# Kernel optimization log

Measured on AMD Instinct MI355X. Metric: run time of the kernel, lower is better.

The kernel has to match this reference:

```python
import jax, jax.numpy as jnp
import numpy as np

B, H, N, D = 4, 4, 2048, 64

def setup_inputs() -> dict:
    key = jax.random.key(0)
    kq, kk, kv, km = jax.random.split(key, 4)
    q = jax.random.normal(kq, (B, H, N, D), dtype=jnp.float32)
    k = jax.random.normal(kk, (B, H, N, D), dtype=jnp.float32)
    v = jax.random.normal(kv, (B, H, N, D), dtype=jnp.float32)
    mask = jax.random.randint(km, (B, N), 0, 2, dtype=jnp.int32)
    return {"q": q, "k": k, "v": v, "mask": mask}

def reference(q, k, v, mask):
    # scores: [B, H, Nq, Nk]
    scale = jnp.asarray(q.shape[-1] ** 0.5, q.dtype)
    scores = jnp.einsum('bhid,bhjd->bhij', q, k) / scale
    neg = jnp.finfo(scores.dtype).min
    m = mask[:, None, None, :]  # [B,1,1,Nk]
    scores = jnp.where(m == 0, neg, scores)
    attention = jax.nn.softmax(scores, axis=-1)
    output = jnp.einsum('bhij,bhjd->bhid', attention, v)
    return (output, attention)
```

## Files before the change

### kernel.cpp

```cpp
#include <hip/hip_runtime.h>

typedef __attribute__((ext_vector_type(8))) short short8;
typedef __attribute__((ext_vector_type(4))) float f32x4;

#define NHEADS 16
#define N_ 2048
#define D_ 64
#define ROWS 16
#define LDP 2056
#define NT 256

__device__ __forceinline__ unsigned short f2b(float f) {
    unsigned u = __float_as_uint(f);
    return (unsigned short)((u + 0x7FFFu + ((u >> 16) & 1u)) >> 16);
}
__device__ __forceinline__ float b2f(unsigned short b) {
    return __uint_as_float(((unsigned)b) << 16);
}

__global__ __launch_bounds__(NT)
void cvt_bf16_kernel(const float4* __restrict__ src, ushort4* __restrict__ dst, int n4)
{
    int i = blockIdx.x * NT + threadIdx.x;
    if (i < n4) {
        float4 v = src[i];
        ushort4 o;
        o.x = f2b(v.x); o.y = f2b(v.y); o.z = f2b(v.z); o.w = f2b(v.w);
        dst[i] = o;
    }
}

__global__ __launch_bounds__(NT)
void vtrans_kernel(const float* __restrict__ v, unsigned short* __restrict__ vt)
{
    __shared__ float tile[64][65];
    const int head = blockIdx.x >> 5;
    const int k0   = (blockIdx.x & 31) * 64;
    const int tid  = threadIdx.x;

    {
        const int i = tid >> 2;
        const int c = tid & 3;
        const float4* v4 = (const float4*)(v + ((size_t)(head * N_ + k0 + i)) * D_);
        #pragma unroll
        for (int u = 0; u < 4; ++u) {
            const int c4 = c + 4 * u;
            float4 val = v4[c4];
            tile[i][c4 * 4 + 0] = val.x;
            tile[i][c4 * 4 + 1] = val.y;
            tile[i][c4 * 4 + 2] = val.z;
            tile[i][c4 * 4 + 3] = val.w;
        }
    }
    __syncthreads();
    {
        const int d  = tid >> 2;
        const int kk = (tid & 3) * 16;
        unsigned short* dst = vt + ((size_t)(head * D_ + d)) * N_ + k0 + kk;
        #pragma unroll
        for (int m4 = 0; m4 < 4; ++m4) {
            ushort4 ov;
            ov.x = f2b(tile[kk + m4 * 4 + 0][d]);
            ov.y = f2b(tile[kk + m4 * 4 + 1][d]);
            ov.z = f2b(tile[kk + m4 * 4 + 2][d]);
            ov.w = f2b(tile[kk + m4 * 4 + 3][d]);
            *(ushort4*)(dst + m4 * 4) = ov;
        }
    }
}

__global__ __launch_bounds__(NT, 2)
void lg_attn(const unsigned short* __restrict__ Qb,
             const unsigned short* __restrict__ Kb,
             const unsigned short* __restrict__ Vt,
             const int* __restrict__ mask,
             float* __restrict__ out,
             float* __restrict__ attn)
{
    __shared__ unsigned short P[ROWS * LDP];
    __shared__ float wred[64];
    __shared__ float rowinv[ROWS];

    const int tid  = threadIdx.x;
    const int w    = tid >> 6;
    const int lane = tid & 63;
    const int quad = lane >> 4;
    const int l16  = lane & 15;

    const int head = blockIdx.x >> 7;
    const int it   = blockIdx.x & 127;
    const int i0   = it * ROWS;
    const int bidx = head >> 2;

    const unsigned short* qrow = Qb + ((size_t)(head * N_ + i0 + l16)) * D_ + quad * 8;
    const short8 a0 = *(const short8*)qrow;
    const short8 a1 = *(const short8*)(qrow + 32);

    const unsigned short* kbase = Kb + (size_t)head * N_ * D_;
    const int* mrow = mask + bidx * N_;

    float bm[4];
    {
        float m4[4] = {-3.4e38f, -3.4e38f, -3.4e38f, -3.4e38f};
        for (int t = 0; t < 32; ++t) {
            const int j0 = (w + 4 * t) * 16;
            const unsigned short* krow = kbase + (size_t)(j0 + l16) * D_ + quad * 8;
            short8 b0 = *(const short8*)krow;
            short8 b1 = *(const short8*)(krow + 32);
            f32x4 c = {0.f, 0.f, 0.f, 0.f};
            c = __builtin_amdgcn_mfma_f32_16x16x32_bf16(a0, b0, c, 0, 0, 0);
            c = __builtin_amdgcn_mfma_f32_16x16x32_bf16(a1, b1, c, 0, 0, 0);
            const int mv = mrow[j0 + l16];
            #pragma unroll
            for (int r = 0; r < 4; ++r) {
                float s = (mv == 0) ? -3.4e38f : c[r] * 0.125f;
                m4[r] = fmaxf(m4[r], s);
            }
        }
        #pragma unroll
        for (int r = 0; r < 4; ++r) {
            #pragma unroll
            for (int off = 1; off < 16; off <<= 1)
                m4[r] = fmaxf(m4[r], __shfl_xor(m4[r], off, 64));
        }
        if (l16 == 0) {
            #pragma unroll
            for (int r = 0; r < 4; ++r) wred[w * 16 + quad * 4 + r] = m4[r];
        }
        __syncthreads();
        #pragma unroll
        for (int r = 0; r < 4; ++r) {
            const int row = quad * 4 + r;
            bm[r] = fmaxf(fmaxf(wred[row], wred[16 + row]),
                          fmaxf(wred[32 + row], wred[48 + row]));
        }
        __syncthreads();
    }

    {
        float s4[4] = {0.f, 0.f, 0.f, 0.f};
        for (int t = 0; t < 32; ++t) {
            const int j0 = (w + 4 * t) * 16;
            const unsigned short* krow = kbase + (size_t)(j0 + l16) * D_ + quad * 8;
            short8 b0 = *(const short8*)krow;
            short8 b1 = *(const short8*)(krow + 32);
            f32x4 c = {0.f, 0.f, 0.f, 0.f};
            c = __builtin_amdgcn_mfma_f32_16x16x32_bf16(a0, b0, c, 0, 0, 0);
            c = __builtin_amdgcn_mfma_f32_16x16x32_bf16(a1, b1, c, 0, 0, 0);
            const int mv = mrow[j0 + l16];
            #pragma unroll
            for (int r = 0; r < 4; ++r) {
                float s = (mv == 0) ? -3.4e38f : c[r] * 0.125f;
                float p = __expf(s - bm[r]);
                s4[r] += p;
                P[(quad * 4 + r) * LDP + j0 + l16] = f2b(p);
            }
        }
        #pragma unroll
        for (int r = 0; r < 4; ++r) {
            #pragma unroll
            for (int off = 1; off < 16; off <<= 1)
                s4[r] += __shfl_xor(s4[r], off, 64);
        }
        if (l16 == 0) {
            #pragma unroll
            for (int r = 0; r < 4; ++r) wred[w * 16 + quad * 4 + r] = s4[r];
        }
        __syncthreads();
        if (w == 0 && l16 == 0) {
            #pragma unroll
            for (int r = 0; r < 4; ++r) {
                const int row = quad * 4 + r;
                const float bs = wred[row] + wred[16 + row] + wred[32 + row] + wred[48 + row];
                rowinv[row] = 1.0f / bs;
            }
        }
        __syncthreads();
    }

    for (int r = 0; r < ROWS; ++r) {
        const float inv = rowinv[r];
        float4* arow = (float4*)(attn + ((size_t)(head * N_ + i0 + r)) * N_);
        for (int c4 = tid; c4 < N_ / 4; c4 += NT) {
            ushort4 tv = *(ushort4*)&P[r * LDP + c4 * 4];
            float4 f;
            f.x = b2f(tv.x) * inv;
            f.y = b2f(tv.y) * inv;
            f.z = b2f(tv.z) * inv;
            f.w = b2f(tv.w) * inv;
            arow[c4] = f;
            tv.x = f2b(f.x); tv.y = f2b(f.y); tv.z = f2b(f.z); tv.w = f2b(f.w);
            *(ushort4*)&P[r * LDP + c4 * 4] = tv;
        }
    }
    __syncthreads();

    {
        const int n0 = w * 16;
        const unsigned short* vbase =
            Vt + ((size_t)(head * D_ + n0 + l16)) * N_ + quad * 8;
        f32x4 o = {0.f, 0.f, 0.f, 0.f};
        for (int kc = 0; kc < 64; ++kc) {
            short8 ap = *(short8*)&P[l16 * LDP + kc * 32 + quad * 8];
            short8 bv = *(const short8*)(vbase + kc * 32);
            o = __builtin_amdgcn_mfma_f32_16x16x32_bf16(ap, bv, o, 0, 0, 0);
        }
        #pragma unroll
        for (int r = 0; r < 4; ++r)
            out[((size_t)(head * N_ + i0 + quad * 4 + r)) * D_ + n0 + l16] = o[r];
    }
}

extern "C" void kernel_launch(void* const* d_in, const int* in_sizes, int n_in,
                              void* d_out, int out_size, void* d_ws, size_t ws_size,
                              hipStream_t stream) {
    const float* q    = (const float*)d_in[0];
    const float* k    = (const float*)d_in[1];
    const float* v    = (const float*)d_in[2];
    const int*   mask = (const int*)d_in[3];

    float* out  = (float*)d_out;
    float* attn = out + (size_t)NHEADS * N_ * D_;

    const size_t elems = (size_t)NHEADS * N_ * D_;
    unsigned short* Qb = (unsigned short*)d_ws;
    unsigned short* Kb = Qb + elems;
    unsigned short* Vt = Kb + elems;

    const int n4 = (int)(elems / 4);
    const int cblocks = (n4 + NT - 1) / NT;
    cvt_bf16_kernel<<<cblocks, NT, 0, stream>>>((const float4*)q, (ushort4*)Qb, n4);
    cvt_bf16_kernel<<<cblocks, NT, 0, stream>>>((const float4*)k, (ushort4*)Kb, n4);
    vtrans_kernel<<<NHEADS * 32, NT, 0, stream>>>(v, Vt);

    lg_attn<<<NHEADS * 128, NT, 0, stream>>>(Qb, Kb, Vt, mask, out, attn);
}
```

Measured before the change: 458.8 us.

## Keep QK scores in registers to avoid recomputing, defer normalization to output

QK^T scores are computed once and held in 32 f32x4 register tiles instead of being recomputed in a second pass. This removes the second round of K loads and MFMAs. The row-sum reduction goes to a separate slice of shared memory, which drops a barrier and the rowinv step. Normalization of the PV output is deferred to the final store, so P no longer needs to be rewritten, and the attention matrix is written with nontemporal stores. Holding 128 extra VGPRs per thread raises register pressure and may reduce occupancy below the two blocks per CU requested by the launch bounds.

```diff
diff --git a/kernel.cpp b/kernel.cpp
--- a/kernel.cpp
+++ b/kernel.cpp
@@ -78,8 +78,7 @@
              float* __restrict__ attn)
 {
     __shared__ unsigned short P[ROWS * LDP];
-    __shared__ float wred[64];
-    __shared__ float rowinv[ROWS];
+    __shared__ float wred[128];
 
     const int tid  = threadIdx.x;
     const int w    = tid >> 6;
@@ -99,30 +98,39 @@
     const unsigned short* kbase = Kb + (size_t)head * N_ * D_;
     const int* mrow = mask + bidx * N_;
 
-    float bm[4];
-    {
-        float m4[4] = {-3.4e38f, -3.4e38f, -3.4e38f, -3.4e38f};
-        for (int t = 0; t < 32; ++t) {
+    f32x4 c[32];
+    #pragma unroll
+    for (int tc = 0; tc < 4; ++tc) {
+        #pragma unroll
+        for (int ti = 0; ti < 8; ++ti) {
+            const int t  = tc * 8 + ti;
             const int j0 = (w + 4 * t) * 16;
             const unsigned short* krow = kbase + (size_t)(j0 + l16) * D_ + quad * 8;
             short8 b0 = *(const short8*)krow;
             short8 b1 = *(const short8*)(krow + 32);
-            f32x4 c = {0.f, 0.f, 0.f, 0.f};
-            c = __builtin_amdgcn_mfma_f32_16x16x32_bf16(a0, b0, c, 0, 0, 0);
-            c = __builtin_amdgcn_mfma_f32_16x16x32_bf16(a1, b1, c, 0, 0, 0);
+            f32x4 cc = {0.f, 0.f, 0.f, 0.f};
+            cc = __builtin_amdgcn_mfma_f32_16x16x32_bf16(a0, b0, cc, 0, 0, 0);
+            cc = __builtin_amdgcn_mfma_f32_16x16x32_bf16(a1, b1, cc, 0, 0, 0);
             const int mv = mrow[j0 + l16];
             #pragma unroll
-            for (int r = 0; r < 4; ++r) {
-                float s = (mv == 0) ? -3.4e38f : c[r] * 0.125f;
-                m4[r] = fmaxf(m4[r], s);
-            }
-        }
-        #pragma unroll
-        for (int r = 0; r < 4; ++r) {
+            for (int r = 0; r < 4; ++r)
+                c[t][r] = (mv == 0) ? -3.4e38f : cc[r];
+        }
+        __builtin_amdgcn_sched_barrier(0);
+    }
+
+    float bm[4];
+    {
+        float m4[4] = {-3.4e38f, -3.4e38f, -3.4e38f, -3.4e38f};
+        #pragma unroll
+        for (int t = 0; t < 32; ++t)
+            #pragma unroll
+            for (int r = 0; r < 4; ++r) m4[r] = fmaxf(m4[r], c[t][r]);
+        #pragma unroll
+        for (int r = 0; r < 4; ++r)
             #pragma unroll
             for (int off = 1; off < 16; off <<= 1)
                 m4[r] = fmaxf(m4[r], __shfl_xor(m4[r], off, 64));
-        }
         if (l16 == 0) {
             #pragma unroll
             for (int r = 0; r < 4; ++r) wred[w * 16 + quad * 4 + r] = m4[r];
@@ -134,80 +142,70 @@
             bm[r] = fmaxf(fmaxf(wred[row], wred[16 + row]),
                           fmaxf(wred[32 + row], wred[48 + row]));
         }
-        __syncthreads();
     }
 
     {
         float s4[4] = {0.f, 0.f, 0.f, 0.f};
+        #pragma unroll
         for (int t = 0; t < 32; ++t) {
             const int j0 = (w + 4 * t) * 16;
-            const unsigned short* krow = kbase + (size_t)(j0 + l16) * D_ + quad * 8;
-            short8 b0 = *(const short8*)krow;
-            short8 b1 = *(const short8*)(krow + 32);
-            f32x4 c = {0.f, 0.f, 0.f, 0.f};
-            c = __builtin_amdgcn_mfma_f32_16x16x32_bf16(a0, b0, c, 0, 0, 0);
-            c = __builtin_amdgcn_mfma_f32_16x16x32_bf16(a1, b1, c, 0, 0, 0);
-            const int mv = mrow[j0 + l16];
             #pragma unroll
             for (int r = 0; r < 4; ++r) {
-                float s = (mv == 0) ? -3.4e38f : c[r] * 0.125f;
-                float p = __expf(s - bm[r]);
+                const float p = __expf((c[t][r] - bm[r]) * 0.125f);
                 s4[r] += p;
                 P[(quad * 4 + r) * LDP + j0 + l16] = f2b(p);
             }
         }
         #pragma unroll
-        for (int r = 0; r < 4; ++r) {
+        for (int r = 0; r < 4; ++r)
             #pragma unroll
             for (int off = 1; off < 16; off <<= 1)
                 s4[r] += __shfl_xor(s4[r], off, 64);
-        }
         if (l16 == 0) {
             #pragma unroll
-            for (int r = 0; r < 4; ++r) wred[w * 16 + quad * 4 + r] = s4[r];
+            for (int r = 0; r < 4; ++r) wred[64 + w * 16 + quad * 4 + r] = s4[r];
         }
         __syncthreads();
-        if (w == 0 && l16 == 0) {
-            #pragma unroll
-            for (int r = 0; r < 4; ++r) {
-                const int row = quad * 4 + r;
-                const float bs = wred[row] + wred[16 + row] + wred[32 + row] + wred[48 + row];
-                rowinv[row] = 1.0f / bs;
+    }
+
+    {
+        const size_t abase = (size_t)(head * N_ + i0) * N_;
+        #pragma unroll 1
+        for (int r = 0; r < ROWS; ++r) {
+            const float s = wred[64 + r] + wred[80 + r] + wred[96 + r] + wred[112 + r];
+            const float inv = 1.0f / s;
+            f32x4* arow = (f32x4*)(attn + abase + (size_t)r * N_);
+            #pragma unroll
+            for (int u = 0; u < 2; ++u) {
+                const int c4 = tid + u * NT;
+                ushort4 tv = *(ushort4*)&P[r * LDP + c4 * 4];
+                f32x4 f;
+                f.x = b2f(tv.x) * inv;
+                f.y = b2f(tv.y) * inv;
+                f.z = b2f(tv.z) * inv;
+                f.w = b2f(tv.w) * inv;
+                __builtin_nontemporal_store(f, &arow[c4]);
             }
         }
-        __syncthreads();
-    }
-
-    for (int r = 0; r < ROWS; ++r) {
-        const float inv = rowinv[r];
-        float4* arow = (float4*)(attn + ((size_t)(head * N_ + i0 + r)) * N_);
-        for (int c4 = tid; c4 < N_ / 4; c4 += NT) {
-            ushort4 tv = *(ushort4*)&P[r * LDP + c4 * 4];
-            float4 f;
-            f.x = b2f(tv.x) * inv;
-            f.y = b2f(tv.y) * inv;
-            f.z = b2f(tv.z) * inv;
-            f.w = b2f(tv.w) * inv;
-            arow[c4] = f;
-            tv.x = f2b(f.x); tv.y = f2b(f.y); tv.z = f2b(f.z); tv.w = f2b(f.w);
-            *(ushort4*)&P[r * LDP + c4 * 4] = tv;
-        }
-    }
-    __syncthreads();
+    }
 
     {
         const int n0 = w * 16;
         const unsigned short* vbase =
             Vt + ((size_t)(head * D_ + n0 + l16)) * N_ + quad * 8;
         f32x4 o = {0.f, 0.f, 0.f, 0.f};
+        #pragma unroll 4
         for (int kc = 0; kc < 64; ++kc) {
             short8 ap = *(short8*)&P[l16 * LDP + kc * 32 + quad * 8];
             short8 bv = *(const short8*)(vbase + kc * 32);
             o = __builtin_amdgcn_mfma_f32_16x16x32_bf16(ap, bv, o, 0, 0, 0);
         }
         #pragma unroll
-        for (int r = 0; r < 4; ++r)
-            out[((size_t)(head * N_ + i0 + quad * 4 + r)) * D_ + n0 + l16] = o[r];
+        for (int r = 0; r < 4; ++r) {
+            const int row = quad * 4 + r;
+            const float s = wred[64 + row] + wred[80 + row] + wred[96 + row] + wred[112 + row];
+            out[((size_t)(head * N_ + i0 + row)) * D_ + n0 + l16] = o[r] / s;
+        }
     }
 }
 
```

Measured after the change: 385.9 us. -15.9%, faster.
